# Performance work log

Measured on AMD Instinct MI355X. Metric: run time of the kernel, lower is better.

The kernel has to match this reference:

```python
import jax, jax.numpy as jnp
import numpy as np

B, D, A, M = 262144, 128, 32, 100


def setup_inputs() -> dict:
    key = jax.random.key(0)
    ks = jax.random.split(key, 8)
    s = 0.05
    return {
        "state": jax.random.normal(ks[0], (B, D), jnp.float32),
        "action": jax.random.normal(ks[1], (B, A), jnp.float32),
        "next_state": jax.random.normal(ks[2], (B, D), jnp.float32),
        "seen": jax.random.normal(ks[3], (M, D), jnp.float32),
        "W1": jax.random.normal(ks[4], (D, D + A), jnp.float32) * s,
        "b1": jnp.zeros((D,), jnp.float32),
        "W2": jax.random.normal(ks[5], (D, D), jnp.float32) * s,
        "b2": jnp.zeros((D,), jnp.float32),
        "Wf": jax.random.normal(ks[6], (D, D), jnp.float32) * s,
        "bf": jnp.zeros((D,), jnp.float32),
    }


def reference(state, action, next_state, seen, W1, b1, W2, b2, Wf, bf):
    # predictor: Linear(D+A -> D) -> ReLU -> Linear(D -> D)   (torch: y = x W^T + b)
    x = jnp.concatenate([state, action], axis=-1)            # [B, D+A]
    h = jax.nn.relu(x @ W1.T + b1)                           # [B, D]
    predicted_next = h @ W2.T + b2                           # [B, D]

    # feature_extractor: Linear(D -> D) -> ReLU
    feat = lambda z: jax.nn.relu(z @ Wf.T + bf)
    features_actual = feat(next_state)                       # [B, D]
    features_pred = feat(predicted_next)                     # [B, D]

    # per-sample MSE prediction error (features_actual detached in original)
    fa_sg = jax.lax.stop_gradient(features_actual)
    pred_error = jnp.mean((features_pred - fa_sg) ** 2, axis=-1)  # [B]

    # 1-NN L2 distance to memory buffer, batched via the ||a-b||^2 expansion
    # (avoids materializing [B, M, D])
    a2 = jnp.sum(features_actual ** 2, axis=-1, keepdims=True)    # [B, 1]
    s2 = jnp.sum(seen ** 2, axis=-1)                              # [M]
    d2 = a2 + s2[None, :] - 2.0 * (features_actual @ seen.T)      # [B, M]
    min_dist = jnp.sqrt(jnp.maximum(jnp.min(d2, axis=-1), 0.0))   # [B]
    novelty = jnp.minimum(1.0, min_dist / 10.0)                   # [B]

    curiosity_reward = pred_error * 0.5 + novelty * 0.5
    return jnp.stack([pred_error, novelty, curiosity_reward])     # [3, B]
```

## Files before the change

kernel.cpp:

```cpp
#include <hip/hip_runtime.h>
#include <math.h>

#define B_TOT 262144

typedef __attribute__((ext_vector_type(8))) short v8s;
typedef __attribute__((ext_vector_type(4))) float v4f;

#define WS_W1 0
#define WS_W2 20480
#define WS_WF 36864
#define WS_SEEN 53248
#define WS_S2_BYTES 135168

__device__ __forceinline__ unsigned short f2bf(float f) {
  union { float f; unsigned u; } cv; cv.f = f;
  unsigned u = cv.u;
  return (unsigned short)((u + 0x7FFFu + ((u >> 16) & 1u)) >> 16);
}
__device__ __forceinline__ float bf2f(unsigned short h) {
  union { unsigned u; float f; } cv; cv.u = ((unsigned)h) << 16;
  return cv.f;
}

__global__ void curiosity_prep(const float* __restrict__ W1, const float* __restrict__ W2,
                               const float* __restrict__ Wf, const float* __restrict__ seen,
                               unsigned short* __restrict__ wsb, float* __restrict__ s2) {
  int bid = blockIdx.x;
  if (bid < 264) {
    int idx = bid * 256 + (int)threadIdx.x;
    if (idx < 20480) {
      int f = idx >> 9, r = idx & 511, L = r >> 3, j = r & 7;
      int t = f / 5, c = f - t * 5;
      int n = t * 16 + (L & 15), k = c * 32 + (L >> 4) * 8 + j;
      wsb[idx] = f2bf(W1[n * 160 + k]);
    } else if (idx < 36864) {
      int e = idx - 20480;
      int f = e >> 9, r = e & 511, L = r >> 3, j = r & 7;
      int t = f >> 2, c = f & 3;
      int n = t * 16 + (L & 15), k = c * 32 + (L >> 4) * 8 + j;
      wsb[idx] = f2bf(W2[n * 128 + k]);
    } else if (idx < 53248) {
      int e = idx - 36864;
      int f = e >> 9, r = e & 511, L = r >> 3, j = r & 7;
      int t = f >> 2, c = f & 3;
      int n = t * 16 + (L & 15), k = c * 32 + (L >> 4) * 8 + j;
      wsb[idx] = f2bf(Wf[n * 128 + k]);
    } else {
      int e = idx - 53248;
      int f = e >> 9, r = e & 511, L = r >> 3, j = r & 7;
      int t = f >> 2, c = f & 3;
      int n = t * 16 + (L & 15), k = c * 32 + (L >> 4) * 8 + j;
      float v = (n < 100) ? seen[n * 128 + k] : 0.f;
      wsb[idx] = f2bf(v);
    }
  } else {
    int wv = (int)threadIdx.x >> 6, lane = (int)threadIdx.x & 63;
    int mm = (bid - 264) * 4 + wv;
    float s;
    if (mm < 100) {
      float v0 = seen[mm * 128 + lane], v1 = seen[mm * 128 + 64 + lane];
      s = v0 * v0 + v1 * v1;
#pragma unroll
      for (int msk = 1; msk < 64; msk <<= 1) s += __shfl_xor(s, msk, 64);
    } else {
      s = 1e30f;
    }
    if (lane == 0) s2[mm] = s;
  }
}

__device__ __forceinline__ void stage16x128(const float* __restrict__ src,
                                            unsigned short* buf, int lane) {
#pragma unroll
  for (int i = 0; i < 8; ++i) {
    int flat = i * 64 + lane;
    int row = flat >> 5, c4 = flat & 31;
    float4 v = *(const float4*)(src + row * 128 + c4 * 4);
    uint2 p;
    p.x = (unsigned)f2bf(v.x) | ((unsigned)f2bf(v.y) << 16);
    p.y = (unsigned)f2bf(v.z) | ((unsigned)f2bf(v.w) << 16);
    *(uint2*)(buf + row * 136 + c4 * 4) = p;
  }
}
__device__ __forceinline__ void stage16x32(const float* __restrict__ src,
                                           unsigned short* buf, int lane) {
#pragma unroll
  for (int i = 0; i < 2; ++i) {
    int flat = i * 64 + lane;
    int row = flat >> 3, c4 = flat & 7;
    float4 v = *(const float4*)(src + row * 32 + c4 * 4);
    uint2 p;
    p.x = (unsigned)f2bf(v.x) | ((unsigned)f2bf(v.y) << 16);
    p.y = (unsigned)f2bf(v.z) | ((unsigned)f2bf(v.w) << 16);
    *(uint2*)(buf + row * 136 + c4 * 4) = p;
  }
}
__device__ __forceinline__ v8s read_frag(const unsigned short* buf, int m, int q, int c) {
  return *(const v8s*)(buf + m * 136 + c * 32 + q * 8);
}
__device__ __forceinline__ v8s wfrag(const unsigned short* __restrict__ wsb,
                                     int base, int fragIdx, int lane) {
  return *(const v8s*)(wsb + base + fragIdx * 512 + lane * 8);
}

__global__ __launch_bounds__(256, 4) void curiosity_main(
    const float* __restrict__ state, const float* __restrict__ action,
    const float* __restrict__ next_state,
    const float* __restrict__ b1, const float* __restrict__ b2,
    const float* __restrict__ bfv,
    const unsigned short* __restrict__ wsb, const float* __restrict__ s2g,
    float* __restrict__ out) {
  __shared__ __attribute__((aligned(16))) unsigned short s_int[4][2][2176];
  __shared__ float s_o[3][128];

  const int tid = (int)threadIdx.x;
  const int w = tid >> 6, lane = tid & 63;
  const int m = lane & 15, q = lane >> 4;
  const int rowblk = (int)blockIdx.x * 128 + w * 32;

  unsigned short* buf[2] = { &s_int[w][0][0], &s_int[w][1][0] };

  v8s a1[2][5];
#pragma unroll
  for (int tt = 0; tt < 2; ++tt) {
    const int gr0 = rowblk + tt * 16;
    stage16x32(action + (size_t)gr0 * 32, buf[tt], lane);
    a1[tt][4] = *(const v8s*)(buf[tt] + m * 136 + q * 8);
    stage16x128(state + (size_t)gr0 * 128, buf[tt], lane);
#pragma unroll
    for (int c = 0; c < 4; ++c) a1[tt][c] = read_frag(buf[tt], m, q, c);
  }

#pragma unroll
  for (int hf = 0; hf < 2; ++hf) {
    v4f acc[2][4] = {};
#pragma unroll
    for (int c = 0; c < 5; ++c) {
#pragma unroll
      for (int tl = 0; tl < 4; ++tl) {
        v8s b = wfrag(wsb, WS_W1, (hf * 4 + tl) * 5 + c, lane);
        acc[0][tl] = __builtin_amdgcn_mfma_f32_16x16x32_bf16(a1[0][c], b, acc[0][tl], 0, 0, 0);
        acc[1][tl] = __builtin_amdgcn_mfma_f32_16x16x32_bf16(a1[1][c], b, acc[1][tl], 0, 0, 0);
      }
    }
#pragma unroll
    for (int tl = 0; tl < 4; ++tl) {
      int tg = hf * 4 + tl;
      float bv = b1[tg * 16 + m];
#pragma unroll
      for (int r = 0; r < 4; ++r) {
        float h0 = fmaxf(acc[0][tl][r] + bv, 0.f);
        float h1 = fmaxf(acc[1][tl][r] + bv, 0.f);
        buf[0][(q * 4 + r) * 136 + tg * 16 + m] = f2bf(h0);
        buf[1][(q * 4 + r) * 136 + tg * 16 + m] = f2bf(h1);
      }
    }
  }

  v8s af[2][4];
#pragma unroll
  for (int tt = 0; tt < 2; ++tt)
#pragma unroll
    for (int c = 0; c < 4; ++c) af[tt][c] = read_frag(buf[tt], m, q, c);
#pragma unroll
  for (int hf = 0; hf < 2; ++hf) {
    v4f acc[2][4] = {};
#pragma unroll
    for (int c = 0; c < 4; ++c) {
#pragma unroll
      for (int tl = 0; tl < 4; ++tl) {
        v8s b = wfrag(wsb, WS_W2, (hf * 4 + tl) * 4 + c, lane);
        acc[0][tl] = __builtin_amdgcn_mfma_f32_16x16x32_bf16(af[0][c], b, acc[0][tl], 0, 0, 0);
        acc[1][tl] = __builtin_amdgcn_mfma_f32_16x16x32_bf16(af[1][c], b, acc[1][tl], 0, 0, 0);
      }
    }
#pragma unroll
    for (int tl = 0; tl < 4; ++tl) {
      int tg = hf * 4 + tl;
      float bv = b2[tg * 16 + m];
#pragma unroll
      for (int r = 0; r < 4; ++r) {
        buf[0][(q * 4 + r) * 136 + tg * 16 + m] = f2bf(acc[0][tl][r] + bv);
        buf[1][(q * 4 + r) * 136 + tg * 16 + m] = f2bf(acc[1][tl][r] + bv);
      }
    }
  }

  v8s a4[2][4], a3[2][4];
#pragma unroll
  for (int tt = 0; tt < 2; ++tt)
#pragma unroll
    for (int c = 0; c < 4; ++c) a4[tt][c] = read_frag(buf[tt], m, q, c);
#pragma unroll
  for (int tt = 0; tt < 2; ++tt) {
    const int gr0 = rowblk + tt * 16;
    stage16x128(next_state + (size_t)gr0 * 128, buf[tt], lane);
#pragma unroll
    for (int c = 0; c < 4; ++c) a3[tt][c] = read_frag(buf[tt], m, q, c);
  }

  float a2s[2][4] = {};
#pragma unroll
  for (int hf = 0; hf < 2; ++hf) {
    v4f acc[2][4] = {};
#pragma unroll
    for (int c = 0; c < 4; ++c) {
#pragma unroll
      for (int tl = 0; tl < 4; ++tl) {
        v8s b = wfrag(wsb, WS_WF, (hf * 4 + tl) * 4 + c, lane);
        acc[0][tl] = __builtin_amdgcn_mfma_f32_16x16x32_bf16(a3[0][c], b, acc[0][tl], 0, 0, 0);
        acc[1][tl] = __builtin_amdgcn_mfma_f32_16x16x32_bf16(a3[1][c], b, acc[1][tl], 0, 0, 0);
      }
    }
#pragma unroll
    for (int tl = 0; tl < 4; ++tl) {
      int tg = hf * 4 + tl;
      float bv = bfv[tg * 16 + m];
#pragma unroll
      for (int tt = 0; tt < 2; ++tt) {
#pragma unroll
        for (int r = 0; r < 4; ++r) {
          float fav = fmaxf(acc[tt][tl][r] + bv, 0.f);
          unsigned short fb = f2bf(fav);
          float fbr = bf2f(fb);
          buf[tt][(q * 4 + r) * 136 + tg * 16 + m] = fb;
          a2s[tt][r] += fbr * fbr;
        }
      }
    }
  }

  float pe[2][4] = {};
#pragma unroll
  for (int hf = 0; hf < 2; ++hf) {
    v4f acc[2][4] = {};
#pragma unroll
    for (int c = 0; c < 4; ++c) {
#pragma unroll
      for (int tl = 0; tl < 4; ++tl) {
        v8s b = wfrag(wsb, WS_WF, (hf * 4 + tl) * 4 + c, lane);
        acc[0][tl] = __builtin_amdgcn_mfma_f32_16x16x32_bf16(a4[0][c], b, acc[0][tl], 0, 0, 0);
        acc[1][tl] = __builtin_amdgcn_mfma_f32_16x16x32_bf16(a4[1][c], b, acc[1][tl], 0, 0, 0);
      }
    }
#pragma unroll
    for (int tl = 0; tl < 4; ++tl) {
      int tg = hf * 4 + tl;
      float bv = bfv[tg * 16 + m];
#pragma unroll
      for (int tt = 0; tt < 2; ++tt) {
#pragma unroll
        for (int r = 0; r < 4; ++r) {
          float fpv = fmaxf(acc[tt][tl][r] + bv, 0.f);
          float fav = bf2f(buf[tt][(q * 4 + r) * 136 + tg * 16 + m]);
          float d = fpv - fav;
          pe[tt][r] += d * d;
        }
      }
    }
  }

#pragma unroll
  for (int tt = 0; tt < 2; ++tt)
#pragma unroll
    for (int r = 0; r < 4; ++r)
#pragma unroll
      for (int msk = 1; msk < 16; msk <<= 1) {
        pe[tt][r] += __shfl_xor(pe[tt][r], msk, 16);
        a2s[tt][r] += __shfl_xor(a2s[tt][r], msk, 16);
      }

  v8s a5[2][4];
#pragma unroll
  for (int tt = 0; tt < 2; ++tt)
#pragma unroll
    for (int c = 0; c < 4; ++c) a5[tt][c] = read_frag(buf[tt], m, q, c);
  float dmin[2][4] = {{3.4e38f, 3.4e38f, 3.4e38f, 3.4e38f},
                      {3.4e38f, 3.4e38f, 3.4e38f, 3.4e38f}};
#pragma unroll
  for (int tl = 0; tl < 7; ++tl) {
    v4f g0 = {}, g1 = {};
#pragma unroll
    for (int c = 0; c < 4; ++c) {
      v8s b = wfrag(wsb, WS_SEEN, tl * 4 + c, lane);
      g0 = __builtin_amdgcn_mfma_f32_16x16x32_bf16(a5[0][c], b, g0, 0, 0, 0);
      g1 = __builtin_amdgcn_mfma_f32_16x16x32_bf16(a5[1][c], b, g1, 0, 0, 0);
    }
    float s2v = s2g[tl * 16 + m];
#pragma unroll
    for (int r = 0; r < 4; ++r) {
      dmin[0][r] = fminf(dmin[0][r], a2s[0][r] + s2v - 2.f * g0[r]);
      dmin[1][r] = fminf(dmin[1][r], a2s[1][r] + s2v - 2.f * g1[r]);
    }
  }
#pragma unroll
  for (int tt = 0; tt < 2; ++tt)
#pragma unroll
    for (int r = 0; r < 4; ++r)
#pragma unroll
      for (int msk = 1; msk < 16; msk <<= 1)
        dmin[tt][r] = fminf(dmin[tt][r], __shfl_xor(dmin[tt][r], msk, 16));

  if (m == 0) {
#pragma unroll
    for (int tt = 0; tt < 2; ++tt)
#pragma unroll
      for (int r = 0; r < 4; ++r) {
        int rl = w * 32 + tt * 16 + q * 4 + r;
        float p = pe[tt][r] * (1.f / 128.f);
        float nov = fminf(1.f, sqrtf(fmaxf(dmin[tt][r], 0.f)) * 0.1f);
        s_o[0][rl] = p;
        s_o[1][rl] = nov;
        s_o[2][rl] = 0.5f * (p + nov);
      }
  }
  __syncthreads();
  const size_t base = (size_t)blockIdx.x * 128;
  for (int idx = tid; idx < 384; idx += 256) {
    int j = idx >> 7, r = idx & 127;
    out[(size_t)j * B_TOT + base + r] = s_o[j][r];
  }
}

extern "C" void kernel_launch(void* const* d_in, const int* in_sizes, int n_in,
                              void* d_out, int out_size, void* d_ws, size_t ws_size,
                              hipStream_t stream) {
  const float* state      = (const float*)d_in[0];
  const float* action     = (const float*)d_in[1];
  const float* next_state = (const float*)d_in[2];
  const float* seen       = (const float*)d_in[3];
  const float* W1         = (const float*)d_in[4];
  const float* b1         = (const float*)d_in[5];
  const float* W2         = (const float*)d_in[6];
  const float* b2         = (const float*)d_in[7];
  const float* Wf         = (const float*)d_in[8];
  const float* bf_        = (const float*)d_in[9];

  unsigned short* wsb = (unsigned short*)d_ws;
  float* s2 = (float*)((char*)d_ws + WS_S2_BYTES);

  curiosity_prep<<<292, 256, 0, stream>>>(W1, W2, Wf, seen, wsb, s2);
  curiosity_main<<<2048, 256, 0, stream>>>(state, action, next_state, b1, b2, bf_,
                                           wsb, s2, (float*)d_out);
}
```

Measured before the change: 385.4 us.

## Batch global loads ahead of MFMA chains and use packed bf16 conversion

Issues all weight-fragment and input loads for each phase into register arrays before the MFMA chain, so global memory latency is overlapped rather than serialized per MFMA. Bias and s2 values are hoisted into registers, and the scalar bit-trick float-to-bf16 rounding is replaced with the packed __float22bfloat162_rn intrinsic. Feature-actual values are kept packed in registers instead of being re-read from LDS. The extra register pressure is acknowledged by lowering launch bounds from 4 to 3 blocks per SM, which may reduce occupancy.

New measurement: 376.1 us. -2.4%, faster.

```diff
diff --git a/kernel.cpp b/kernel.cpp
--- a/kernel.cpp
+++ b/kernel.cpp
@@ -1,4 +1,5 @@
 #include <hip/hip_runtime.h>
+#include <hip/hip_bf16.h>
 #include <math.h>
 
 #define B_TOT 262144
@@ -20,6 +21,12 @@
 __device__ __forceinline__ float bf2f(unsigned short h) {
   union { unsigned u; float f; } cv; cv.u = ((unsigned)h) << 16;
   return cv.f;
+}
+__device__ __forceinline__ unsigned f2bf2(float x, float y) {
+  float2 f; f.x = x; f.y = y;
+  __hip_bfloat162 h = __float22bfloat162_rn(f);
+  union { __hip_bfloat162 h; unsigned u; } cv; cv.h = h;
+  return cv.u;
 }
 
 __global__ void curiosity_prep(const float* __restrict__ W1, const float* __restrict__ W2,
@@ -71,28 +78,36 @@
 
 __device__ __forceinline__ void stage16x128(const float* __restrict__ src,
                                             unsigned short* buf, int lane) {
+  float4 v[8];
 #pragma unroll
   for (int i = 0; i < 8; ++i) {
     int flat = i * 64 + lane;
-    int row = flat >> 5, c4 = flat & 31;
-    float4 v = *(const float4*)(src + row * 128 + c4 * 4);
+    v[i] = *(const float4*)(src + (flat >> 5) * 128 + (flat & 31) * 4);
+  }
+#pragma unroll
+  for (int i = 0; i < 8; ++i) {
+    int flat = i * 64 + lane;
     uint2 p;
-    p.x = (unsigned)f2bf(v.x) | ((unsigned)f2bf(v.y) << 16);
-    p.y = (unsigned)f2bf(v.z) | ((unsigned)f2bf(v.w) << 16);
-    *(uint2*)(buf + row * 136 + c4 * 4) = p;
+    p.x = f2bf2(v[i].x, v[i].y);
+    p.y = f2bf2(v[i].z, v[i].w);
+    *(uint2*)(buf + (flat >> 5) * 136 + (flat & 31) * 4) = p;
   }
 }
 __device__ __forceinline__ void stage16x32(const float* __restrict__ src,
                                            unsigned short* buf, int lane) {
+  float4 v[2];
 #pragma unroll
   for (int i = 0; i < 2; ++i) {
     int flat = i * 64 + lane;
-    int row = flat >> 3, c4 = flat & 7;
-    float4 v = *(const float4*)(src + row * 32 + c4 * 4);
+    v[i] = *(const float4*)(src + (flat >> 3) * 32 + (flat & 7) * 4);
+  }
+#pragma unroll
+  for (int i = 0; i < 2; ++i) {
+    int flat = i * 64 + lane;
     uint2 p;
-    p.x = (unsigned)f2bf(v.x) | ((unsigned)f2bf(v.y) << 16);
-    p.y = (unsigned)f2bf(v.z) | ((unsigned)f2bf(v.w) << 16);
-    *(uint2*)(buf + row * 136 + c4 * 4) = p;
+    p.x = f2bf2(v[i].x, v[i].y);
+    p.y = f2bf2(v[i].z, v[i].w);
+    *(uint2*)(buf + (flat >> 3) * 136 + (flat & 7) * 4) = p;
   }
 }
 __device__ __forceinline__ v8s read_frag(const unsigned short* buf, int m, int q, int c) {
@@ -103,7 +118,7 @@
   return *(const v8s*)(wsb + base + fragIdx * 512 + lane * 8);
 }
 
-__global__ __launch_bounds__(256, 4) void curiosity_main(
+__global__ __launch_bounds__(256, 3) void curiosity_main(
     const float* __restrict__ state, const float* __restrict__ action,
     const float* __restrict__ next_state,
     const float* __restrict__ b1, const float* __restrict__ b2,
@@ -120,143 +135,189 @@
 
   unsigned short* buf[2] = { &s_int[w][0][0], &s_int[w][1][0] };
 
+  float bv1[8];
+#pragma unroll
+  for (int tg = 0; tg < 8; ++tg) bv1[tg] = b1[tg * 16 + m];
+
   v8s a1[2][5];
-#pragma unroll
-  for (int tt = 0; tt < 2; ++tt) {
-    const int gr0 = rowblk + tt * 16;
-    stage16x32(action + (size_t)gr0 * 32, buf[tt], lane);
-    a1[tt][4] = *(const v8s*)(buf[tt] + m * 136 + q * 8);
-    stage16x128(state + (size_t)gr0 * 128, buf[tt], lane);
-#pragma unroll
-    for (int c = 0; c < 4; ++c) a1[tt][c] = read_frag(buf[tt], m, q, c);
-  }
+  stage16x32(action + (size_t)(rowblk) * 32, buf[0], lane);
+  stage16x32(action + (size_t)(rowblk + 16) * 32, buf[1], lane);
+  a1[0][4] = *(const v8s*)(buf[0] + m * 136 + q * 8);
+  a1[1][4] = *(const v8s*)(buf[1] + m * 136 + q * 8);
+  stage16x128(state + (size_t)(rowblk) * 128, buf[0], lane);
+  stage16x128(state + (size_t)(rowblk + 16) * 128, buf[1], lane);
+#pragma unroll
+  for (int c = 0; c < 4; ++c) {
+    a1[0][c] = read_frag(buf[0], m, q, c);
+    a1[1][c] = read_frag(buf[1], m, q, c);
+  }
+
+  float bv2[8];
+#pragma unroll
+  for (int tg = 0; tg < 8; ++tg) bv2[tg] = b2[tg * 16 + m];
 
 #pragma unroll
   for (int hf = 0; hf < 2; ++hf) {
+    v8s bfr[20];
+#pragma unroll
+    for (int c = 0; c < 5; ++c)
+#pragma unroll
+      for (int tl = 0; tl < 4; ++tl)
+        bfr[c * 4 + tl] = wfrag(wsb, WS_W1, (hf * 4 + tl) * 5 + c, lane);
     v4f acc[2][4] = {};
 #pragma unroll
-    for (int c = 0; c < 5; ++c) {
+    for (int c = 0; c < 5; ++c)
 #pragma unroll
       for (int tl = 0; tl < 4; ++tl) {
-        v8s b = wfrag(wsb, WS_W1, (hf * 4 + tl) * 5 + c, lane);
-        acc[0][tl] = __builtin_amdgcn_mfma_f32_16x16x32_bf16(a1[0][c], b, acc[0][tl], 0, 0, 0);
-        acc[1][tl] = __builtin_amdgcn_mfma_f32_16x16x32_bf16(a1[1][c], b, acc[1][tl], 0, 0, 0);
-      }
-    }
+        acc[0][tl] = __builtin_amdgcn_mfma_f32_16x16x32_bf16(a1[0][c], bfr[c * 4 + tl], acc[0][tl], 0, 0, 0);
+        acc[1][tl] = __builtin_amdgcn_mfma_f32_16x16x32_bf16(a1[1][c], bfr[c * 4 + tl], acc[1][tl], 0, 0, 0);
+      }
 #pragma unroll
     for (int tl = 0; tl < 4; ++tl) {
       int tg = hf * 4 + tl;
-      float bv = b1[tg * 16 + m];
-#pragma unroll
-      for (int r = 0; r < 4; ++r) {
-        float h0 = fmaxf(acc[0][tl][r] + bv, 0.f);
-        float h1 = fmaxf(acc[1][tl][r] + bv, 0.f);
-        buf[0][(q * 4 + r) * 136 + tg * 16 + m] = f2bf(h0);
-        buf[1][(q * 4 + r) * 136 + tg * 16 + m] = f2bf(h1);
-      }
+      float bv = bv1[tg];
+#pragma unroll
+      for (int tt = 0; tt < 2; ++tt)
+#pragma unroll
+        for (int r = 0; r < 4; r += 2) {
+          unsigned p = f2bf2(fmaxf(acc[tt][tl][r] + bv, 0.f),
+                             fmaxf(acc[tt][tl][r + 1] + bv, 0.f));
+          buf[tt][(q * 4 + r) * 136 + tg * 16 + m] = (unsigned short)p;
+          buf[tt][(q * 4 + r + 1) * 136 + tg * 16 + m] = (unsigned short)(p >> 16);
+        }
     }
   }
 
   v8s af[2][4];
 #pragma unroll
-  for (int tt = 0; tt < 2; ++tt)
-#pragma unroll
-    for (int c = 0; c < 4; ++c) af[tt][c] = read_frag(buf[tt], m, q, c);
+  for (int c = 0; c < 4; ++c) {
+    af[0][c] = read_frag(buf[0], m, q, c);
+    af[1][c] = read_frag(buf[1], m, q, c);
+  }
+  float bvf[8];
+#pragma unroll
+  for (int tg = 0; tg < 8; ++tg) bvf[tg] = bfv[tg * 16 + m];
+
 #pragma unroll
   for (int hf = 0; hf < 2; ++hf) {
+    v8s bfr[16];
+#pragma unroll
+    for (int c = 0; c < 4; ++c)
+#pragma unroll
+      for (int tl = 0; tl < 4; ++tl)
+        bfr[c * 4 + tl] = wfrag(wsb, WS_W2, (hf * 4 + tl) * 4 + c, lane);
     v4f acc[2][4] = {};
 #pragma unroll
-    for (int c = 0; c < 4; ++c) {
+    for (int c = 0; c < 4; ++c)
 #pragma unroll
       for (int tl = 0; tl < 4; ++tl) {
-        v8s b = wfrag(wsb, WS_W2, (hf * 4 + tl) * 4 + c, lane);
-        acc[0][tl] = __builtin_amdgcn_mfma_f32_16x16x32_bf16(af[0][c], b, acc[0][tl], 0, 0, 0);
-        acc[1][tl] = __builtin_amdgcn_mfma_f32_16x16x32_bf16(af[1][c], b, acc[1][tl], 0, 0, 0);
-      }
-    }
+        acc[0][tl] = __builtin_amdgcn_mfma_f32_16x16x32_bf16(af[0][c], bfr[c * 4 + tl], acc[0][tl], 0, 0, 0);
+        acc[1][tl] = __builtin_amdgcn_mfma_f32_16x16x32_bf16(af[1][c], bfr[c * 4 + tl], acc[1][tl], 0, 0, 0);
+      }
 #pragma unroll
     for (int tl = 0; tl < 4; ++tl) {
       int tg = hf * 4 + tl;
-      float bv = b2[tg * 16 + m];
-#pragma unroll
-      for (int r = 0; r < 4; ++r) {
-        buf[0][(q * 4 + r) * 136 + tg * 16 + m] = f2bf(acc[0][tl][r] + bv);
-        buf[1][(q * 4 + r) * 136 + tg * 16 + m] = f2bf(acc[1][tl][r] + bv);
-      }
+      float bv = bv2[tg];
+#pragma unroll
+      for (int tt = 0; tt < 2; ++tt)
+#pragma unroll
+        for (int r = 0; r < 4; r += 2) {
+          unsigned p = f2bf2(acc[tt][tl][r] + bv, acc[tt][tl][r + 1] + bv);
+          buf[tt][(q * 4 + r) * 136 + tg * 16 + m] = (unsigned short)p;
+          buf[tt][(q * 4 + r + 1) * 136 + tg * 16 + m] = (unsigned short)(p >> 16);
+        }
     }
   }
 
   v8s a4[2][4], a3[2][4];
 #pragma unroll
-  for (int tt = 0; tt < 2; ++tt)
-#pragma unroll
-    for (int c = 0; c < 4; ++c) a4[tt][c] = read_frag(buf[tt], m, q, c);
-#pragma unroll
-  for (int tt = 0; tt < 2; ++tt) {
-    const int gr0 = rowblk + tt * 16;
-    stage16x128(next_state + (size_t)gr0 * 128, buf[tt], lane);
-#pragma unroll
-    for (int c = 0; c < 4; ++c) a3[tt][c] = read_frag(buf[tt], m, q, c);
-  }
-
+  for (int c = 0; c < 4; ++c) {
+    a4[0][c] = read_frag(buf[0], m, q, c);
+    a4[1][c] = read_frag(buf[1], m, q, c);
+  }
+  stage16x128(next_state + (size_t)(rowblk) * 128, buf[0], lane);
+  stage16x128(next_state + (size_t)(rowblk + 16) * 128, buf[1], lane);
+#pragma unroll
+  for (int c = 0; c < 4; ++c) {
+    a3[0][c] = read_frag(buf[0], m, q, c);
+    a3[1][c] = read_frag(buf[1], m, q, c);
+  }
+
+  float s2v[7];
+#pragma unroll
+  for (int tl = 0; tl < 7; ++tl) s2v[tl] = s2g[tl * 16 + m];
+
+  unsigned fa_pk[2][16];
   float a2s[2][4] = {};
 #pragma unroll
   for (int hf = 0; hf < 2; ++hf) {
+    v8s bfr[16];
+#pragma unroll
+    for (int c = 0; c < 4; ++c)
+#pragma unroll
+      for (int tl = 0; tl < 4; ++tl)
+        bfr[c * 4 + tl] = wfrag(wsb, WS_WF, (hf * 4 + tl) * 4 + c, lane);
     v4f acc[2][4] = {};
 #pragma unroll
-    for (int c = 0; c < 4; ++c) {
+    for (int c = 0; c < 4; ++c)
 #pragma unroll
       for (int tl = 0; tl < 4; ++tl) {
-        v8s b = wfrag(wsb, WS_WF, (hf * 4 + tl) * 4 + c, lane);
-        acc[0][tl] = __builtin_amdgcn_mfma_f32_16x16x32_bf16(a3[0][c], b, acc[0][tl], 0, 0, 0);
-        acc[1][tl] = __builtin_amdgcn_mfma_f32_16x16x32_bf16(a3[1][c], b, acc[1][tl], 0, 0, 0);
-      }
-    }
+        acc[0][tl] = __builtin_amdgcn_mfma_f32_16x16x32_bf16(a3[0][c], bfr[c * 4 + tl], acc[0][tl], 0, 0, 0);
+        acc[1][tl] = __builtin_amdgcn_mfma_f32_16x16x32_bf16(a3[1][c], bfr[c * 4 + tl], acc[1][tl], 0, 0, 0);
+      }
 #pragma unroll
     for (int tl = 0; tl < 4; ++tl) {
       int tg = hf * 4 + tl;
-      float bv = bfv[tg * 16 + m];
-#pragma unroll
-      for (int tt = 0; tt < 2; ++tt) {
-#pragma unroll
-        for (int r = 0; r < 4; ++r) {
-          float fav = fmaxf(acc[tt][tl][r] + bv, 0.f);
-          unsigned short fb = f2bf(fav);
-          float fbr = bf2f(fb);
-          buf[tt][(q * 4 + r) * 136 + tg * 16 + m] = fb;
-          a2s[tt][r] += fbr * fbr;
+      float bv = bvf[tg];
+#pragma unroll
+      for (int tt = 0; tt < 2; ++tt)
+#pragma unroll
+        for (int rp = 0; rp < 2; ++rp) {
+          int r = rp * 2;
+          unsigned p = f2bf2(fmaxf(acc[tt][tl][r] + bv, 0.f),
+                             fmaxf(acc[tt][tl][r + 1] + bv, 0.f));
+          fa_pk[hf][tl * 4 + tt * 2 + rp] = p;
+          buf[tt][(q * 4 + r) * 136 + tg * 16 + m] = (unsigned short)p;
+          buf[tt][(q * 4 + r + 1) * 136 + tg * 16 + m] = (unsigned short)(p >> 16);
+          float flo = bf2f((unsigned short)p), fhi = bf2f((unsigned short)(p >> 16));
+          a2s[tt][r] += flo * flo;
+          a2s[tt][r + 1] += fhi * fhi;
         }
-      }
     }
   }
 
   float pe[2][4] = {};
 #pragma unroll
   for (int hf = 0; hf < 2; ++hf) {
+    v8s bfr[16];
+#pragma unroll
+    for (int c = 0; c < 4; ++c)
+#pragma unroll
+      for (int tl = 0; tl < 4; ++tl)
+        bfr[c * 4 + tl] = wfrag(wsb, WS_WF, (hf * 4 + tl) * 4 + c, lane);
     v4f acc[2][4] = {};
 #pragma unroll
-    for (int c = 0; c < 4; ++c) {
+    for (int c = 0; c < 4; ++c)
 #pragma unroll
       for (int tl = 0; tl < 4; ++tl) {
-        v8s b = wfrag(wsb, WS_WF, (hf * 4 + tl) * 4 + c, lane);
-        acc[0][tl] = __builtin_amdgcn_mfma_f32_16x16x32_bf16(a4[0][c], b, acc[0][tl], 0, 0, 0);
-        acc[1][tl] = __builtin_amdgcn_mfma_f32_16x16x32_bf16(a4[1][c], b, acc[1][tl], 0, 0, 0);
-      }
-    }
+        acc[0][tl] = __builtin_amdgcn_mfma_f32_16x16x32_bf16(a4[0][c], bfr[c * 4 + tl], acc[0][tl], 0, 0, 0);
+        acc[1][tl] = __builtin_amdgcn_mfma_f32_16x16x32_bf16(a4[1][c], bfr[c * 4 + tl], acc[1][tl], 0, 0, 0);
+      }
 #pragma unroll
     for (int tl = 0; tl < 4; ++tl) {
       int tg = hf * 4 + tl;
-      float bv = bfv[tg * 16 + m];
-#pragma unroll
-      for (int tt = 0; tt < 2; ++tt) {
-#pragma unroll
-        for (int r = 0; r < 4; ++r) {
-          float fpv = fmaxf(acc[tt][tl][r] + bv, 0.f);
-          float fav = bf2f(buf[tt][(q * 4 + r) * 136 + tg * 16 + m]);
-          float d = fpv - fav;
-          pe[tt][r] += d * d;
+      float bv = bvf[tg];
+#pragma unroll
+      for (int tt = 0; tt < 2; ++tt)
+#pragma unroll
+        for (int rp = 0; rp < 2; ++rp) {
+          int r = rp * 2;
+          unsigned p = fa_pk[hf][tl * 4 + tt * 2 + rp];
+          float d0 = fmaxf(acc[tt][tl][r] + bv, 0.f) - bf2f((unsigned short)p);
+          float d1 = fmaxf(acc[tt][tl][r + 1] + bv, 0.f) - bf2f((unsigned short)(p >> 16));
+          pe[tt][r] += d0 * d0;
+          pe[tt][r + 1] += d1 * d1;
         }
-      }
     }
   }
 
@@ -272,25 +333,56 @@
 
   v8s a5[2][4];
 #pragma unroll
-  for (int tt = 0; tt < 2; ++tt)
-#pragma unroll
-    for (int c = 0; c < 4; ++c) a5[tt][c] = read_frag(buf[tt], m, q, c);
+  for (int c = 0; c < 4; ++c) {
+    a5[0][c] = read_frag(buf[0], m, q, c);
+    a5[1][c] = read_frag(buf[1], m, q, c);
+  }
   float dmin[2][4] = {{3.4e38f, 3.4e38f, 3.4e38f, 3.4e38f},
                       {3.4e38f, 3.4e38f, 3.4e38f, 3.4e38f}};
-#pragma unroll
-  for (int tl = 0; tl < 7; ++tl) {
-    v4f g0 = {}, g1 = {};
-#pragma unroll
-    for (int c = 0; c < 4; ++c) {
-      v8s b = wfrag(wsb, WS_SEEN, tl * 4 + c, lane);
-      g0 = __builtin_amdgcn_mfma_f32_16x16x32_bf16(a5[0][c], b, g0, 0, 0, 0);
-      g1 = __builtin_amdgcn_mfma_f32_16x16x32_bf16(a5[1][c], b, g1, 0, 0, 0);
-    }
-    float s2v = s2g[tl * 16 + m];
-#pragma unroll
-    for (int r = 0; r < 4; ++r) {
-      dmin[0][r] = fminf(dmin[0][r], a2s[0][r] + s2v - 2.f * g0[r]);
-      dmin[1][r] = fminf(dmin[1][r], a2s[1][r] + s2v - 2.f * g1[r]);
+  {
+    v8s bfr[16];
+#pragma unroll
+    for (int tl = 0; tl < 4; ++tl)
+#pragma unroll
+      for (int c = 0; c < 4; ++c)
+        bfr[tl * 4 + c] = wfrag(wsb, WS_SEEN, tl * 4 + c, lane);
+#pragma unroll
+    for (int tl = 0; tl < 4; ++tl) {
+      v4f g0 = {}, g1 = {};
+#pragma unroll
+      for (int c = 0; c < 4; ++c) {
+        g0 = __builtin_amdgcn_mfma_f32_16x16x32_bf16(a5[0][c], bfr[tl * 4 + c], g0, 0, 0, 0);
+        g1 = __builtin_amdgcn_mfma_f32_16x16x32_bf16(a5[1][c], bfr[tl * 4 + c], g1, 0, 0, 0);
+      }
+      float s2x = s2v[tl];
+#pragma unroll
+      for (int r = 0; r < 4; ++r) {
+        dmin[0][r] = fminf(dmin[0][r], a2s[0][r] + s2x - 2.f * g0[r]);
+        dmin[1][r] = fminf(dmin[1][r], a2s[1][r] + s2x - 2.f * g1[r]);
+      }
+    }
+  }
+  {
+    v8s bfr[12];
+#pragma unroll
+    for (int tl = 0; tl < 3; ++tl)
+#pragma unroll
+      for (int c = 0; c < 4; ++c)
+        bfr[tl * 4 + c] = wfrag(wsb, WS_SEEN, (tl + 4) * 4 + c, lane);
+#pragma unroll
+    for (int tl = 0; tl < 3; ++tl) {
+      v4f g0 = {}, g1 = {};
+#pragma unroll
+      for (int c = 0; c < 4; ++c) {
+        g0 = __builtin_amdgcn_mfma_f32_16x16x32_bf16(a5[0][c], bfr[tl * 4 + c], g0, 0, 0, 0);
+        g1 = __builtin_amdgcn_mfma_f32_16x16x32_bf16(a5[1][c], bfr[tl * 4 + c], g1, 0, 0, 0);
+      }
+      float s2x = s2v[tl + 4];
+#pragma unroll
+      for (int r = 0; r < 4; ++r) {
+        dmin[0][r] = fminf(dmin[0][r], a2s[0][r] + s2x - 2.f * g0[r]);
+        dmin[1][r] = fminf(dmin[1][r], a2s[1][r] + s2x - 2.f * g1[r]);
+      }
     }
   }
 #pragma unroll
```
